# Performance work log

Measured on AMD Instinct MI355X. Metric: run time of the kernel, lower is better.

Reference implementation:

```python
import jax, jax.numpy as jnp
import numpy as np

N, C, D, DOUT = 1024, 64, 16, 16   # nodes, channels, irreps_in dim (lmax=3), irreps_out dim
K3, K2, K1 = 16, 8, 4              # CG basis path counts per correlation order
NUM_ELEMENTS = 10


def _sym_basis(key, shape, sym_axes):
    """Random stand-in for e3nn reduced-CG U tensors: symmetrized over input axes."""
    u = jax.random.normal(key, shape, dtype=jnp.float32)
    acc = jnp.zeros(shape, jnp.float32)
    import itertools
    perms = list(itertools.permutations(sym_axes))
    for p in perms:
        order = list(range(len(shape)))
        for a, b in zip(sym_axes, p):
            order[a] = b
        acc = acc + jnp.transpose(u, order)
    return 0.05 * acc / len(perms)


def setup_inputs() -> dict:
    key = jax.random.key(0)
    ks = jax.random.split(key, 8)
    x = jax.random.normal(ks[0], (N, C, D), dtype=jnp.float32)
    indices = jax.random.randint(ks[1], (N,), 0, NUM_ELEMENTS, dtype=jnp.int32)
    w1 = jax.random.normal(ks[2], (NUM_ELEMENTS, K1, C), dtype=jnp.float32)
    w2 = jax.random.normal(ks[3], (NUM_ELEMENTS, K2, C), dtype=jnp.float32)
    w3 = jax.random.normal(ks[4], (NUM_ELEMENTS, K3, C), dtype=jnp.float32)
    U1 = _sym_basis(ks[5], (DOUT, D, K1), (1,))
    U2 = _sym_basis(ks[6], (DOUT, D, D, K2), (1, 2))
    U3 = _sym_basis(ks[7], (DOUT, D, D, D, K3), (1, 2, 3))
    return {"x": x, "indices": indices, "w1": w1, "w2": w2, "w3": w3,
            "U1": U1, "U2": U2, "U3": U3}


def reference(x, indices, w1, w2, w3, U1, U2, U3):
    # Per-node element selection of basis weights (replaces one-hot einsum 'ekc,be->bkc')
    w3s = w3[indices]  # [N, K3, C]
    w2s = w2[indices]  # [N, K2, C]
    w1s = w1[indices]  # [N, K1, C]

    # correlation 3: contract highest-order CG basis with weights and one copy of x
    # out[b,c,o,i,j] = sum_{l,k} U3[o,i,j,l,k] * w3s[b,k,c] * x[b,c,l]
    out = jnp.einsum('oijlk,bkc,bcl->bcoij', U3, w3s, x)

    # correlation 2: add weighted basis, contract one more copy of x
    out = out + jnp.einsum('oijk,bkc->bcoij', U2, w2s)
    out = jnp.einsum('bcoij,bcj->bcoi', out, x)

    # correlation 1: add weighted basis, contract last copy of x
    out = out + jnp.einsum('oik,bkc->bcoi', U1, w1s)
    out = jnp.einsum('bcoi,bci->bco', out, x)  # [N, C, DOUT]
    return out
```

## Files before the change

kernel.cpp:

```cpp
#include <hip/hip_runtime.h>
#include <hip/hip_bf16.h>

#define NCH 64
#define NEL 10
#define NCHUNK 192
#define NSTEP 48
#define NROWS 24576

#define WS_OFFS   0
#define WS_LIST   1024
#define WS_WALLT  8192
#define WS_UPACK  65536
#define WS_W      2097152

typedef __attribute__((ext_vector_type(8))) short  short8v;
typedef __attribute__((ext_vector_type(4))) float  float4v;
typedef __attribute__((ext_vector_type(4))) int    int4v;

__host__ __device__ constexpr int PJF(int p) { int j = 0; while (p >= j + 1) { p -= j + 1; ++j; } return j; }
__host__ __device__ constexpr int PIF(int p) { int j = 0; while (p >= j + 1) { p -= j + 1; ++j; } return p; }
__host__ __device__ constexpr int PJH(int p) { int j = 8; while (p >= j + 1) { p -= j + 1; ++j; } return j; }
__host__ __device__ constexpr int PIH(int p) { int j = 8; while (p >= j + 1) { p -= j + 1; ++j; } return p; }

__device__ __forceinline__ unsigned int f_to_bf16u(float f) {
  union { float f; unsigned int i; } v; v.f = f;
  unsigned int x = v.i;
  unsigned int r = (x + 0x7fffu + ((x >> 16) & 1u)) >> 16;
  return r & 0xffffu;
}

__global__ __launch_bounds__(256) void k_pack(const float* __restrict__ U3,
                                              const float* __restrict__ U2,
                                              const float* __restrict__ U1,
                                              const float* __restrict__ w3,
                                              const float* __restrict__ w2,
                                              const float* __restrict__ w1,
                                              const int* __restrict__ idx,
                                              unsigned short* __restrict__ Upack,
                                              unsigned short* __restrict__ wallT,
                                              int* __restrict__ ws_offs,
                                              int* __restrict__ ws_list) {
  int b = blockIdx.x;
  int t = threadIdx.x;
  if (b == 404) {
    __shared__ int cnt[NEL];
    __shared__ int base[NEL + 1];
    if (t < NEL) cnt[t] = 0;
    __syncthreads();
    int mye[4], myp[4];
#pragma unroll
    for (int k = 0; k < 4; ++k) {
      int n = t + k * 256;
      int e = idx[n];
      mye[k] = e;
      myp[k] = atomicAdd(&cnt[e], 1);
    }
    __syncthreads();
    if (t == 0) {
      int a = 0;
      for (int i = 0; i < NEL; ++i) { base[i] = a; a += cnt[i]; }
      base[NEL] = a;
    }
    __syncthreads();
#pragma unroll
    for (int k = 0; k < 4; ++k) ws_list[base[mye[k]] + myp[k]] = t + k * 256;
    if (t <= NEL) ws_offs[t] = base[t];
  } else if (b < 384) {
    int tau = b * 256 + t;
    int row = tau >> 2, kq = tau & 3;
    int o = row / 1536;
    int rem = row - o * 1536;
    int u = rem >> 3, jj = rem & 7;
    int n = u ^ (o & 7);
    float v[8] = {0.f, 0.f, 0.f, 0.f, 0.f, 0.f, 0.f, 0.f};
    if (n < 172) {
      int ci, cj, h;
      if (n < 72) { int p = n >> 1; h = n & 1; int j = 0; while (p >= j + 1) { p -= j + 1; ++j; } ci = p; cj = j; }
      else        { int p = n - 72; h = 1;     int j = 8; while (p >= j + 1) { p -= j + 1; ++j; } ci = p; cj = j; }
      int l = h * 8 + jj;
      if (kq < 2 && l >= cj) {
        const float* line = U3 + ((((size_t)o * 16 + ci) * 16 + cj) * 16 + l) * 16 + kq * 8;
        float4 q0 = *(const float4*)line;
        float4 q1 = *(const float4*)(line + 4);
        float mult = (ci == cj) ? (cj == l ? 1.f : 3.f) : (cj == l ? 3.f : 6.f);
        v[0] = q0.x * mult; v[1] = q0.y * mult; v[2] = q0.z * mult; v[3] = q0.w * mult;
        v[4] = q1.x * mult; v[5] = q1.y * mult; v[6] = q1.z * mult; v[7] = q1.w * mult;
      }
    } else {
      int r = (n - 172) * 8 + jj;
      if (kq == 2 && r < 136) {
        int p = r, i2 = 0; while (p >= 16 - i2) { p -= 16 - i2; ++i2; }
        int a = i2, bb = i2 + p;
        const float* line = U2 + (((o * 16 + a) * 16) + bb) * 8;
        float4 q0 = *(const float4*)line;
        float4 q1 = *(const float4*)(line + 4);
        float sc = (a == bb) ? 1.f : 2.f;
        v[0] = q0.x * sc; v[1] = q0.y * sc; v[2] = q0.z * sc; v[3] = q0.w * sc;
        v[4] = q1.x * sc; v[5] = q1.y * sc; v[6] = q1.z * sc; v[7] = q1.w * sc;
      } else if (kq == 3 && r >= 136 && r < 152) {
        int a = r - 136;
        float4 q0 = *(const float4*)(U1 + (o * 16 + a) * 4);
        v[0] = q0.x; v[1] = q0.y; v[2] = q0.z; v[3] = q0.w;
      }
    }
    uint4 st;
    st.x = f_to_bf16u(v[0]) | (f_to_bf16u(v[1]) << 16);
    st.y = f_to_bf16u(v[2]) | (f_to_bf16u(v[3]) << 16);
    st.z = f_to_bf16u(v[4]) | (f_to_bf16u(v[5]) << 16);
    st.w = f_to_bf16u(v[6]) | (f_to_bf16u(v[7]) << 16);
    *(uint4*)(Upack + (size_t)row * 32 + kq * 8) = st;
  } else {
    int tau = (b - 384) * 256 + t;
    if (tau < 5120) {
      int kg = tau & 7, ecw = tau >> 3;
      int e = ecw >> 6, c = ecw & 63;
      unsigned int pk[2];
#pragma unroll
      for (int hh = 0; hh < 2; ++hh) {
        int k0 = kg * 4 + hh * 2;
        float f0, f1;
        int k = k0;
        f0 = (k < 16) ? w3[(e * 16 + k) * NCH + c]
           : (k < 24) ? w2[(e * 8 + (k - 16)) * NCH + c]
           : (k < 28) ? w1[(e * 4 + (k - 24)) * NCH + c] : 0.f;
        k = k0 + 1;
        f1 = (k < 16) ? w3[(e * 16 + k) * NCH + c]
           : (k < 24) ? w2[(e * 8 + (k - 16)) * NCH + c]
           : (k < 28) ? w1[(e * 4 + (k - 24)) * NCH + c] : 0.f;
        pk[hh] = f_to_bf16u(f0) | (f_to_bf16u(f1) << 16);
      }
      uint2 st = {pk[0], pk[1]};
      *(uint2*)(wallT + (size_t)ecw * 32 + kg * 4) = st;
    }
  }
}

__global__ __launch_bounds__(256) void k_bgemm(const unsigned short* __restrict__ Upack,
                                               const unsigned short* __restrict__ wallT,
                                               unsigned short* __restrict__ W) {
  __shared__ char sLT[4][2048];
  int b = blockIdx.x;
  int e = b / 96, rb = b - e * 96;
  int t = threadIdx.x, w = t >> 6, lane = t & 63;
  int rc = lane & 15, g = lane >> 4;
  int c = w * 16 + rc;
  short8v bv = *(const short8v*)(wallT + ((size_t)(e * 64 + c)) * 32 + g * 8);
  char* wb = &sLT[w][0];
  int c_r = lane >> 2, q = lane & 3;
  int woff = rc * 128 + ((g * 8) ^ ((rc & 7) << 4));
  int roff0 = c_r * 128 + ((q * 16) ^ ((c_r & 7) << 4));
  int roff1 = c_r * 128 + (((64 + q * 16)) ^ ((c_r & 7) << 4));
  unsigned short* gcol = W + ((size_t)(e * 64 + w * 16 + c_r)) * NROWS + rb * 256;

#pragma unroll 1
  for (int grp = 0; grp < 4; ++grp) {
#pragma unroll
    for (int rt2 = 0; rt2 < 4; ++rt2) {
      int row0 = (rb * 16 + grp * 4 + rt2) * 16;
      short8v av = *(const short8v*)(Upack + (size_t)(row0 + rc) * 32 + g * 8);
      float4v acc = {0.f, 0.f, 0.f, 0.f};
      acc = __builtin_amdgcn_mfma_f32_16x16x32_bf16(av, bv, acc, 0, 0, 0);
      unsigned int lo, hi;
      asm("v_cvt_pk_bf16_f32 %0, %1, %2" : "=v"(lo) : "v"(acc[0]), "v"(acc[1]));
      asm("v_cvt_pk_bf16_f32 %0, %1, %2" : "=v"(hi) : "v"(acc[2]), "v"(acc[3]));
      uint2 pk = {lo, hi};
      *(uint2*)(wb + (woff ^ (rt2 * 32))) = pk;
    }
    uint4 u0 = *(const uint4*)(wb + roff0);
    uint4 u1 = *(const uint4*)(wb + roff1);
    unsigned short* gp = gcol + grp * 64;
    *(uint4*)(gp + q * 8) = u0;
    *(uint4*)(gp + 32 + q * 8) = u1;
  }
}

#define PACK_MFMA(M0, M1, M2, M3, M4, M5, M6, M7, KK, ACC) { \
  int b0, b1, b2, b3; \
  asm("v_cvt_pk_bf16_f32 %0, %1, %2" : "=v"(b0) : "v"(M0), "v"(M1)); \
  asm("v_cvt_pk_bf16_f32 %0, %1, %2" : "=v"(b1) : "v"(M2), "v"(M3)); \
  asm("v_cvt_pk_bf16_f32 %0, %1, %2" : "=v"(b2) : "v"(M4), "v"(M5)); \
  asm("v_cvt_pk_bf16_f32 %0, %1, %2" : "=v"(b3) : "v"(M6), "v"(M7)); \
  int4v ai = {b0, b1, b2, b3}; \
  short8v av = __builtin_bit_cast(short8v, ai); \
  short8v bv = *(const short8v*)(((KK) & 1 ? bpO : bpE) + ((KK) >> 1) * 128); \
  ACC = __builtin_amdgcn_mfma_f32_16x16x32_bf16(av, bv, ACC, 0, 0, 0); \
}

#define FULL_STEP(KK, ACC) { \
  constexpr int iA = PIF(2 * (KK)), jA = PJF(2 * (KK)); \
  constexpr int iB = PIF(2 * (KK) + 1), jB = PJF(2 * (KK) + 1); \
  float xxA = xr[iA] * xr[jA]; \
  float xxB = xr[iB] * xr[jB]; \
  float xx = selOdd ? xxB : xxA; \
  PACK_MFMA(xx * xsF[0], xx * xsF[1], xx * xsF[2], xx * xsF[3], \
            xx * xsF[4], xx * xsF[5], xx * xsF[6], xx * xsF[7], KK, ACC) \
}

#define H1_STEP(KK, ACC) { \
  constexpr int q = 4 * ((KK) - 18); \
  constexpr int i0 = PIH(q), j0 = PJH(q); \
  constexpr int i1 = PIH(q + 1), j1 = PJH(q + 1); \
  constexpr int i2 = PIH(q + 2), j2 = PJH(q + 2); \
  constexpr int i3 = PIH(q + 3), j3 = PJH(q + 3); \
  float xx0 = xr[i0] * xr[j0], xx1 = xr[i1] * xr[j1]; \
  float xx2 = xr[i2] * xr[j2], xx3 = xr[i3] * xr[j3]; \
  float xxE = selG1 ? xx1 : xx0; \
  float xxO = selG1 ? xx3 : xx2; \
  float xx = selOdd ? xxO : xxE; \
  PACK_MFMA(xx * xr[8], xx * xr[9], xx * xr[10], xx * xr[11], \
            xx * xr[12], xx * xr[13], xx * xr[14], xx * xr[15], KK, ACC) \
}

#define TAIL_STEP(KK, ACC) { \
  float mv[8]; \
  _Pragma("unroll") \
  for (int jj = 0; jj < 8; ++jj) { \
    int spec = sT[((KK) - 43) * 32 + g * 8 + jj]; \
    mv[jj] = sXw[spec & 31] * sXw[(spec >> 8) & 31]; \
  } \
  PACK_MFMA(mv[0], mv[1], mv[2], mv[3], mv[4], mv[5], mv[6], mv[7], KK, ACC) \
}

__global__ __launch_bounds__(512, 4) void k_main(const float* __restrict__ x,
                                                 const int* __restrict__ offs,
                                                 const int* __restrict__ list,
                                                 const unsigned short* __restrict__ W,
                                                 float* __restrict__ out) {
  __shared__ unsigned short sB[16 * NCHUNK * 8];
  __shared__ float sX[8][16][18];
  __shared__ int sT[160];
  int t = threadIdx.x;
  int w = t >> 6, lane = t & 63;
  int rc = lane & 15;
  int g = lane >> 4;
  bool selOdd = g >= 2;
  bool selG1 = g & 1;

  int ec = blockIdx.x;
  int e = ec >> 6, c = ec & 63;

  {
    const uint4* Wg4 = (const uint4*)(W + (size_t)ec * NROWS);
    uint4* sB4 = (uint4*)sB;
#pragma unroll
    for (int s = 0; s < 6; ++s) sB4[t + 512 * s] = Wg4[t + 512 * s];
  }
  if (t < 160) {
    int r = t, a, b;
    if (r < 136) { int p = r, i2 = 0; while (p >= 16 - i2) { p -= 16 - i2; ++i2; } a = i2; b = i2 + p; }
    else if (r < 152) { a = r - 136; b = 16; }
    else { a = 17; b = 17; }
    sT[r] = a | (b << 8);
  }
  __syncthreads();

  float* sXw = &sX[w][rc][0];
  int off = offs[e], nb = offs[e + 1] - off;
  int nt = (nb + 15) >> 4;
  int r2 = (rc >> 2) & 1;
  const char* bpE = (const char*)sB + rc * 3072 + ((g ^ (rc & 3)) + 4 * r2) * 16;
  const char* bpO = (const char*)sB + rc * 3072 + ((g ^ (rc & 3)) + 4 * (1 ^ r2)) * 16;

  for (int tile = w; tile < nt; tile += 8) {
    int m = tile * 16 + rc;
    int node = list[off + (m < nb ? m : nb - 1)];
    float xr[16];
    {
      const float4* xp = (const float4*)(x + ((size_t)node * NCH + c) * 16);
      float4 q0 = xp[0], q1 = xp[1], q2 = xp[2], q3 = xp[3];
      xr[0] = q0.x; xr[1] = q0.y; xr[2] = q0.z; xr[3] = q0.w;
      xr[4] = q1.x; xr[5] = q1.y; xr[6] = q1.z; xr[7] = q1.w;
      xr[8] = q2.x; xr[9] = q2.y; xr[10] = q2.z; xr[11] = q2.w;
      xr[12] = q3.x; xr[13] = q3.y; xr[14] = q3.z; xr[15] = q3.w;
    }
    float xsF[8];
#pragma unroll
    for (int j = 0; j < 8; ++j) xsF[j] = selG1 ? xr[8 + j] : xr[j];
    if (g == 0) {
#pragma unroll
      for (int l = 0; l < 16; ++l) sXw[l] = xr[l];
      sXw[16] = 1.f; sXw[17] = 0.f;
    }

    float4v acc0 = {0.f, 0.f, 0.f, 0.f};
    float4v acc1 = {0.f, 0.f, 0.f, 0.f};
#define S2F(K) FULL_STEP(K, acc0) FULL_STEP((K) + 1, acc1)
#define S2H(K) H1_STEP(K, acc0) H1_STEP((K) + 1, acc1)
    S2F(0) S2F(2) S2F(4) S2F(6) S2F(8) S2F(10) S2F(12) S2F(14) S2F(16)
    S2H(18) S2H(20) S2H(22) S2H(24) S2H(26) S2H(28) S2H(30) S2H(32)
    S2H(34) S2H(36) S2H(38) S2H(40)
    H1_STEP(42, acc0)
    TAIL_STEP(43, acc1)
    TAIL_STEP(44, acc0) TAIL_STEP(45, acc1)
    TAIL_STEP(46, acc0) TAIL_STEP(47, acc1)
    float4v accs = acc0 + acc1;

#pragma unroll
    for (int r3 = 0; r3 < 4; ++r3) {
      int row = g * 4 + r3;
      int mrow = tile * 16 + row;
      if (mrow < nb) {
        int nd = __shfl(node, row);
        out[((size_t)nd * NCH + c) * 16 + rc] = accs[r3];
      }
    }
  }
}

extern "C" void kernel_launch(void* const* d_in, const int* in_sizes, int n_in,
                              void* d_out, int out_size, void* d_ws, size_t ws_size,
                              hipStream_t stream) {
  (void)in_sizes; (void)n_in; (void)out_size; (void)ws_size;
  const float* x   = (const float*)d_in[0];
  const int*   idx = (const int*)d_in[1];
  const float* w1  = (const float*)d_in[2];
  const float* w2  = (const float*)d_in[3];
  const float* w3  = (const float*)d_in[4];
  const float* U1  = (const float*)d_in[5];
  const float* U2  = (const float*)d_in[6];
  const float* U3  = (const float*)d_in[7];
  float* out = (float*)d_out;
  char* ws = (char*)d_ws;
  int* ws_offs = (int*)(ws + WS_OFFS);
  int* ws_list = (int*)(ws + WS_LIST);
  unsigned short* wallT = (unsigned short*)(ws + WS_WALLT);
  unsigned short* Upack = (unsigned short*)(ws + WS_UPACK);
  unsigned short* W     = (unsigned short*)(ws + WS_W);

  hipLaunchKernelGGL(k_pack, dim3(405), dim3(256), 0, stream, U3, U2, U1, w3, w2, w1,
                     idx, Upack, wallT, ws_offs, ws_list);
  hipLaunchKernelGGL(k_bgemm, dim3(960), dim3(256), 0, stream, Upack, wallT, W);
  hipLaunchKernelGGL(k_main, dim3(640), dim3(512), 0, stream, x, ws_offs, ws_list, W, out);
}
```

Baseline: 44.51 us.

## Fuse U/weight packing into the basis GEMM kernel via shared memory

Merges the separate packing kernel into the per-element GEMM kernel. Each block now builds its 256-row bf16 slice of the CG basis and the element's weight tile directly in LDS, then runs the MFMA contraction from LDS. The element-sort work moves to an extra block. This removes one kernel launch and the global round-trip of the packed buffers. In exchange, every element's blocks recompute the same U packing, ten times redundantly, and each block uses more LDS.

```diff
diff --git a/kernel.cpp b/kernel.cpp
--- a/kernel.cpp
+++ b/kernel.cpp
@@ -9,8 +9,6 @@
 
 #define WS_OFFS   0
 #define WS_LIST   1024
-#define WS_WALLT  8192
-#define WS_UPACK  65536
 #define WS_W      2097152
 
 typedef __attribute__((ext_vector_type(8))) short  short8v;
@@ -29,22 +27,25 @@
   return r & 0xffffu;
 }
 
-__global__ __launch_bounds__(256) void k_pack(const float* __restrict__ U3,
-                                              const float* __restrict__ U2,
-                                              const float* __restrict__ U1,
-                                              const float* __restrict__ w3,
-                                              const float* __restrict__ w2,
-                                              const float* __restrict__ w1,
-                                              const int* __restrict__ idx,
-                                              unsigned short* __restrict__ Upack,
-                                              unsigned short* __restrict__ wallT,
-                                              int* __restrict__ ws_offs,
-                                              int* __restrict__ ws_list) {
+__global__ __launch_bounds__(256) void k_bgemm(const float* __restrict__ U3,
+                                               const float* __restrict__ U2,
+                                               const float* __restrict__ U1,
+                                               const float* __restrict__ w3,
+                                               const float* __restrict__ w2,
+                                               const float* __restrict__ w1,
+                                               const int* __restrict__ idx,
+                                               unsigned short* __restrict__ W,
+                                               int* __restrict__ ws_offs,
+                                               int* __restrict__ ws_list) {
+  __shared__ unsigned short sU[256 * 32];
+  __shared__ unsigned short sWt[64 * 32];
+  __shared__ char sLT[4][2048];
+  __shared__ int cnt[NEL];
+  __shared__ int base[NEL + 1];
   int b = blockIdx.x;
   int t = threadIdx.x;
-  if (b == 404) {
-    __shared__ int cnt[NEL];
-    __shared__ int base[NEL + 1];
+
+  if (b == 960) {
     if (t < NEL) cnt[t] = 0;
     __syncthreads();
     int mye[4], myp[4];
@@ -65,86 +66,84 @@
 #pragma unroll
     for (int k = 0; k < 4; ++k) ws_list[base[mye[k]] + myp[k]] = t + k * 256;
     if (t <= NEL) ws_offs[t] = base[t];
-  } else if (b < 384) {
-    int tau = b * 256 + t;
-    int row = tau >> 2, kq = tau & 3;
+    return;
+  }
+
+  int e = b / 96, rb = b - e * 96;
+
+  {
+    int row = rb * 256 + t;
     int o = row / 1536;
     int rem = row - o * 1536;
     int u = rem >> 3, jj = rem & 7;
     int n = u ^ (o & 7);
-    float v[8] = {0.f, 0.f, 0.f, 0.f, 0.f, 0.f, 0.f, 0.f};
-    if (n < 172) {
-      int ci, cj, h;
-      if (n < 72) { int p = n >> 1; h = n & 1; int j = 0; while (p >= j + 1) { p -= j + 1; ++j; } ci = p; cj = j; }
-      else        { int p = n - 72; h = 1;     int j = 8; while (p >= j + 1) { p -= j + 1; ++j; } ci = p; cj = j; }
-      int l = h * 8 + jj;
-      if (kq < 2 && l >= cj) {
-        const float* line = U3 + ((((size_t)o * 16 + ci) * 16 + cj) * 16 + l) * 16 + kq * 8;
-        float4 q0 = *(const float4*)line;
-        float4 q1 = *(const float4*)(line + 4);
-        float mult = (ci == cj) ? (cj == l ? 1.f : 3.f) : (cj == l ? 3.f : 6.f);
-        v[0] = q0.x * mult; v[1] = q0.y * mult; v[2] = q0.z * mult; v[3] = q0.w * mult;
-        v[4] = q1.x * mult; v[5] = q1.y * mult; v[6] = q1.z * mult; v[7] = q1.w * mult;
+#pragma unroll
+    for (int kq = 0; kq < 4; ++kq) {
+      float v[8] = {0.f, 0.f, 0.f, 0.f, 0.f, 0.f, 0.f, 0.f};
+      if (n < 172) {
+        int ci, cj, h;
+        if (n < 72) { int p = n >> 1; h = n & 1; int j = 0; while (p >= j + 1) { p -= j + 1; ++j; } ci = p; cj = j; }
+        else        { int p = n - 72; h = 1;     int j = 8; while (p >= j + 1) { p -= j + 1; ++j; } ci = p; cj = j; }
+        int l = h * 8 + jj;
+        if (kq < 2 && l >= cj) {
+          const float* line = U3 + ((((size_t)o * 16 + ci) * 16 + cj) * 16 + l) * 16 + kq * 8;
+          float4 q0 = *(const float4*)line;
+          float4 q1 = *(const float4*)(line + 4);
+          float mult = (ci == cj) ? (cj == l ? 1.f : 3.f) : (cj == l ? 3.f : 6.f);
+          v[0] = q0.x * mult; v[1] = q0.y * mult; v[2] = q0.z * mult; v[3] = q0.w * mult;
+          v[4] = q1.x * mult; v[5] = q1.y * mult; v[6] = q1.z * mult; v[7] = q1.w * mult;
+        }
+      } else {
+        int r = (n - 172) * 8 + jj;
+        if (kq == 2 && r < 136) {
+          int p = r, i2 = 0; while (p >= 16 - i2) { p -= 16 - i2; ++i2; }
+          int a = i2, bb = i2 + p;
+          const float* line = U2 + (((o * 16 + a) * 16) + bb) * 8;
+          float4 q0 = *(const float4*)line;
+          float4 q1 = *(const float4*)(line + 4);
+          float sc = (a == bb) ? 1.f : 2.f;
+          v[0] = q0.x * sc; v[1] = q0.y * sc; v[2] = q0.z * sc; v[3] = q0.w * sc;
+          v[4] = q1.x * sc; v[5] = q1.y * sc; v[6] = q1.z * sc; v[7] = q1.w * sc;
+        } else if (kq == 3 && r >= 136 && r < 152) {
+          int a = r - 136;
+          float4 q0 = *(const float4*)(U1 + (o * 16 + a) * 4);
+          v[0] = q0.x; v[1] = q0.y; v[2] = q0.z; v[3] = q0.w;
+        }
       }
-    } else {
-      int r = (n - 172) * 8 + jj;
-      if (kq == 2 && r < 136) {
-        int p = r, i2 = 0; while (p >= 16 - i2) { p -= 16 - i2; ++i2; }
-        int a = i2, bb = i2 + p;
-        const float* line = U2 + (((o * 16 + a) * 16) + bb) * 8;
-        float4 q0 = *(const float4*)line;
-        float4 q1 = *(const float4*)(line + 4);
-        float sc = (a == bb) ? 1.f : 2.f;
-        v[0] = q0.x * sc; v[1] = q0.y * sc; v[2] = q0.z * sc; v[3] = q0.w * sc;
-        v[4] = q1.x * sc; v[5] = q1.y * sc; v[6] = q1.z * sc; v[7] = q1.w * sc;
-      } else if (kq == 3 && r >= 136 && r < 152) {
-        int a = r - 136;
-        float4 q0 = *(const float4*)(U1 + (o * 16 + a) * 4);
-        v[0] = q0.x; v[1] = q0.y; v[2] = q0.z; v[3] = q0.w;
-      }
-    }
-    uint4 st;
-    st.x = f_to_bf16u(v[0]) | (f_to_bf16u(v[1]) << 16);
-    st.y = f_to_bf16u(v[2]) | (f_to_bf16u(v[3]) << 16);
-    st.z = f_to_bf16u(v[4]) | (f_to_bf16u(v[5]) << 16);
-    st.w = f_to_bf16u(v[6]) | (f_to_bf16u(v[7]) << 16);
-    *(uint4*)(Upack + (size_t)row * 32 + kq * 8) = st;
-  } else {
-    int tau = (b - 384) * 256 + t;
-    if (tau < 5120) {
-      int kg = tau & 7, ecw = tau >> 3;
-      int e = ecw >> 6, c = ecw & 63;
-      unsigned int pk[2];
-#pragma unroll
-      for (int hh = 0; hh < 2; ++hh) {
-        int k0 = kg * 4 + hh * 2;
-        float f0, f1;
-        int k = k0;
-        f0 = (k < 16) ? w3[(e * 16 + k) * NCH + c]
-           : (k < 24) ? w2[(e * 8 + (k - 16)) * NCH + c]
-           : (k < 28) ? w1[(e * 4 + (k - 24)) * NCH + c] : 0.f;
-        k = k0 + 1;
-        f1 = (k < 16) ? w3[(e * 16 + k) * NCH + c]
-           : (k < 24) ? w2[(e * 8 + (k - 16)) * NCH + c]
-           : (k < 28) ? w1[(e * 4 + (k - 24)) * NCH + c] : 0.f;
-        pk[hh] = f_to_bf16u(f0) | (f_to_bf16u(f1) << 16);
-      }
-      uint2 st = {pk[0], pk[1]};
-      *(uint2*)(wallT + (size_t)ecw * 32 + kg * 4) = st;
-    }
-  }
-}
-
-__global__ __launch_bounds__(256) void k_bgemm(const unsigned short* __restrict__ Upack,
-                                               const unsigned short* __restrict__ wallT,
-                                               unsigned short* __restrict__ W) {
-  __shared__ char sLT[4][2048];
-  int b = blockIdx.x;
-  int e = b / 96, rb = b - e * 96;
-  int t = threadIdx.x, w = t >> 6, lane = t & 63;
+      uint4 st;
+      st.x = f_to_bf16u(v[0]) | (f_to_bf16u(v[1]) << 16);
+      st.y = f_to_bf16u(v[2]) | (f_to_bf16u(v[3]) << 16);
+      st.z = f_to_bf16u(v[4]) | (f_to_bf16u(v[5]) << 16);
+      st.w = f_to_bf16u(v[6]) | (f_to_bf16u(v[7]) << 16);
+      *(uint4*)(&sU[t * 32 + kq * 8]) = st;
+    }
+  }
+  {
+    int c = t & 63, kg = t >> 6;
+    unsigned int pk[4];
+#pragma unroll
+    for (int hh = 0; hh < 4; ++hh) {
+      int k0 = kg * 8 + hh * 2;
+      float f0, f1;
+      int k = k0;
+      f0 = (k < 16) ? w3[(e * 16 + k) * NCH + c]
+         : (k < 24) ? w2[(e * 8 + (k - 16)) * NCH + c]
+         : (k < 28) ? w1[(e * 4 + (k - 24)) * NCH + c] : 0.f;
+      k = k0 + 1;
+      f1 = (k < 16) ? w3[(e * 16 + k) * NCH + c]
+         : (k < 24) ? w2[(e * 8 + (k - 16)) * NCH + c]
+         : (k < 28) ? w1[(e * 4 + (k - 24)) * NCH + c] : 0.f;
+      pk[hh] = f_to_bf16u(f0) | (f_to_bf16u(f1) << 16);
+    }
+    uint4 st = {pk[0], pk[1], pk[2], pk[3]};
+    *(uint4*)(&sWt[c * 32 + kg * 8]) = st;
+  }
+  __syncthreads();
+
+  int w = t >> 6, lane = t & 63;
   int rc = lane & 15, g = lane >> 4;
   int c = w * 16 + rc;
-  short8v bv = *(const short8v*)(wallT + ((size_t)(e * 64 + c)) * 32 + g * 8);
+  short8v bv = *(const short8v*)(sWt + c * 32 + g * 8);
   char* wb = &sLT[w][0];
   int c_r = lane >> 2, q = lane & 3;
   int woff = rc * 128 + ((g * 8) ^ ((rc & 7) << 4));
@@ -156,8 +155,8 @@
   for (int grp = 0; grp < 4; ++grp) {
 #pragma unroll
     for (int rt2 = 0; rt2 < 4; ++rt2) {
-      int row0 = (rb * 16 + grp * 4 + rt2) * 16;
-      short8v av = *(const short8v*)(Upack + (size_t)(row0 + rc) * 32 + g * 8);
+      int rowL = (grp * 4 + rt2) * 16 + rc;
+      short8v av = *(const short8v*)(sU + rowL * 32 + g * 8);
       float4v acc = {0.f, 0.f, 0.f, 0.f};
       acc = __builtin_amdgcn_mfma_f32_16x16x32_bf16(av, bv, acc, 0, 0, 0);
       unsigned int lo, hi;
@@ -323,12 +322,9 @@
   char* ws = (char*)d_ws;
   int* ws_offs = (int*)(ws + WS_OFFS);
   int* ws_list = (int*)(ws + WS_LIST);
-  unsigned short* wallT = (unsigned short*)(ws + WS_WALLT);
-  unsigned short* Upack = (unsigned short*)(ws + WS_UPACK);
-  unsigned short* W     = (unsigned short*)(ws + WS_W);
-
-  hipLaunchKernelGGL(k_pack, dim3(405), dim3(256), 0, stream, U3, U2, U1, w3, w2, w1,
-                     idx, Upack, wallT, ws_offs, ws_list);
-  hipLaunchKernelGGL(k_bgemm, dim3(960), dim3(256), 0, stream, Upack, wallT, W);
+  unsigned short* W = (unsigned short*)(ws + WS_W);
+
+  hipLaunchKernelGGL(k_bgemm, dim3(961), dim3(256), 0, stream, U3, U2, U1, w3, w2, w1,
+                     idx, W, ws_offs, ws_list);
   hipLaunchKernelGGL(k_main, dim3(640), dim3(512), 0, stream, x, ws_offs, ws_list, W, out);
 }
```

After: 41.55 us. 1.07x faster.
